# Optimization experiments

Hardware: AMD Instinct MI355X
Metric: run time of the kernel (lower is better)

## Reference

```python
import jax, jax.numpy as jnp
import numpy as np

E = 8192      # number of original edges -> artificial nodes
N = 2048      # number of original graph nodes (id range)
C_IN = 128
C_OUT = 128
NEG_SLOPE = 0.2


def setup_inputs() -> dict:
    key = jax.random.key(0)
    k1, k2, k3, k4, k5 = jax.random.split(key, 5)
    x = jax.random.normal(k1, (E, C_IN), dtype=jnp.float32)
    edge_index = jax.random.randint(k2, (2, E), 0, N, dtype=jnp.int64)
    # GATConv params (heads=1): linear weight, attention vectors, bias
    W = jax.random.normal(k3, (C_IN, C_OUT), dtype=jnp.float32) / np.sqrt(C_IN)
    att_src = jax.random.normal(k4, (C_OUT,), dtype=jnp.float32) / np.sqrt(C_OUT)
    att_dst = jax.random.normal(k5, (C_OUT,), dtype=jnp.float32) / np.sqrt(C_OUT)
    bias = jnp.zeros((C_OUT,), dtype=jnp.float32)
    return {"x": x, "edge_index": edge_index, "W": W,
            "att_src": att_src, "att_dst": att_dst, "bias": bias}


def reference(x, edge_index, W, att_src, att_dst, bias):
    # --- line-graph construction (vectorized version of the O(E^2) loop) ---
    s = edge_index[0]  # [E] source node of each original edge
    d = edge_index[1]  # [E] target node of each original edge
    share = ((s[:, None] == s[None, :]) | (s[:, None] == d[None, :]) |
             (d[:, None] == s[None, :]) | (d[:, None] == d[None, :]))  # [E,E]
    eye = jnp.eye(x.shape[0], dtype=bool)
    # original loop only adds pairs i != j (symmetrically); GATConv then adds self loops
    adj = (share & ~eye) | eye  # adj[i, j]: message j -> i allowed

    # --- GATConv (heads=1, concat) over the dense line-graph adjacency ---
    h = x @ W                       # [E, C_OUT]
    a_src = h @ att_src             # [E] per-source attention logit
    a_dst = h @ att_dst             # [E] per-target attention logit
    scores = a_dst[:, None] + a_src[None, :]          # [E,E], row=target, col=source
    scores = jax.nn.leaky_relu(scores, NEG_SLOPE)
    scores = jnp.where(adj, scores, -jnp.inf)
    alpha = jax.nn.softmax(scores, axis=1)            # softmax over source edges per target
    out = alpha @ h + bias          # [E, C_OUT]
    return out
```

## Files before the change

kernel.cpp:

```cpp
#include <hip/hip_runtime.h>

#define E 8192
#define NNODE 2048
#define C 128
#define CAPN 32
#define NIDX 8
#define NPI (NNODE / NIDX)
#define RPB 32
#define NGEMM (E / RPB)

typedef unsigned int u32;
typedef unsigned long long u64;

__global__ __launch_bounds__(256) void gat_prep(
    const float* __restrict__ x, const float* __restrict__ W,
    const float* __restrict__ att_s, const float* __restrict__ att_d,
    const float* __restrict__ bias, const int* __restrict__ ei,
    float* __restrict__ h, float* __restrict__ asrc, float* __restrict__ adst,
    int* __restrict__ packed, int* __restrict__ cnt, int* __restrict__ nlist)
{
    __shared__ __align__(16) float smem[8192];
    const int tid = threadIdx.x;

    if (blockIdx.x < NIDX) {
        int* lcnt = (int*)smem;
        const int lo = (int)blockIdx.x * NPI;
        if (tid < NPI) lcnt[tid] = 0;
        __syncthreads();
        for (int g = tid; g < E; g += 256) {
            const int s = ei[g], d = ei[E + g];
            if ((g >> 10) == (int)blockIdx.x)
                packed[g] = (s << 16) | d;
            const int sl = s - lo, dl = d - lo;
            if ((unsigned)sl < NPI) {
                const int slot = atomicAdd(&lcnt[sl], 1);
                if (slot < CAPN) nlist[s * CAPN + slot] = g;
            }
            if (d != s && (unsigned)dl < NPI) {
                const int slot = atomicAdd(&lcnt[dl], 1);
                if (slot < CAPN) nlist[d * CAPN + slot] = g;
            }
        }
        __syncthreads();
        if (tid < NPI) cnt[lo + tid] = lcnt[tid];
        return;
    }

    float* xs = smem;
    float* wt = smem + 4096;
    const int lane = tid & 63, wv = tid >> 6;
    const int row0 = ((int)blockIdx.x - NIDX) * RPB;

    #pragma unroll
    for (int u = 0; u < 4; ++u) {
        const int f = tid + u * 256;
        *reinterpret_cast<float4*>(&xs[f * 4]) =
            *reinterpret_cast<const float4*>(&x[(size_t)row0 * C + f * 4]);
    }

    float a0x = 0.f, a0y = 0.f, a1x = 0.f, a1y = 0.f;
    float a2x = 0.f, a2y = 0.f, a3x = 0.f, a3y = 0.f;
    float a4x = 0.f, a4y = 0.f, a5x = 0.f, a5y = 0.f;
    float a6x = 0.f, a6y = 0.f, a7x = 0.f, a7y = 0.f;
    const float* xw = xs + (wv * 8) * C;

    for (int kt = 0; kt < 4; ++kt) {
        __syncthreads();
        #pragma unroll
        for (int u = 0; u < 4; ++u) {
            const int f = tid + u * 256;
            *reinterpret_cast<float4*>(&wt[f * 4]) =
                *reinterpret_cast<const float4*>(&W[(size_t)kt * 32 * C + f * 4]);
        }
        __syncthreads();
        const int kb = kt * 32;
        #pragma unroll
        for (int k4 = 0; k4 < 8; ++k4) {
            float4 v0 = *reinterpret_cast<const float4*>(&xw[0 * C + kb + k4 * 4]);
            float4 v1 = *reinterpret_cast<const float4*>(&xw[1 * C + kb + k4 * 4]);
            float4 v2 = *reinterpret_cast<const float4*>(&xw[2 * C + kb + k4 * 4]);
            float4 v3 = *reinterpret_cast<const float4*>(&xw[3 * C + kb + k4 * 4]);
            float4 v4 = *reinterpret_cast<const float4*>(&xw[4 * C + kb + k4 * 4]);
            float4 v5 = *reinterpret_cast<const float4*>(&xw[5 * C + kb + k4 * 4]);
            float4 v6 = *reinterpret_cast<const float4*>(&xw[6 * C + kb + k4 * 4]);
            float4 v7 = *reinterpret_cast<const float4*>(&xw[7 * C + kb + k4 * 4]);
            const float2 w0 = *reinterpret_cast<const float2*>(&wt[(k4 * 4 + 0) * C + 2 * lane]);
            const float2 w1 = *reinterpret_cast<const float2*>(&wt[(k4 * 4 + 1) * C + 2 * lane]);
            const float2 w2 = *reinterpret_cast<const float2*>(&wt[(k4 * 4 + 2) * C + 2 * lane]);
            const float2 w3 = *reinterpret_cast<const float2*>(&wt[(k4 * 4 + 3) * C + 2 * lane]);
#define K4FMA(V, AX, AY)                                     \
            AX = fmaf(V.x, w0.x, AX); AY = fmaf(V.x, w0.y, AY); \
            AX = fmaf(V.y, w1.x, AX); AY = fmaf(V.y, w1.y, AY); \
            AX = fmaf(V.z, w2.x, AX); AY = fmaf(V.z, w2.y, AY); \
            AX = fmaf(V.w, w3.x, AX); AY = fmaf(V.w, w3.y, AY);
            K4FMA(v0, a0x, a0y) K4FMA(v1, a1x, a1y)
            K4FMA(v2, a2x, a2y) K4FMA(v3, a3x, a3y)
            K4FMA(v4, a4x, a4y) K4FMA(v5, a5x, a5y)
            K4FMA(v6, a6x, a6y) K4FMA(v7, a7x, a7y)
#undef K4FMA
        }
    }

    const float2 asv = *reinterpret_cast<const float2*>(att_s + 2 * lane);
    const float2 adv = *reinterpret_cast<const float2*>(att_d + 2 * lane);
    const float2 bv  = *reinterpret_cast<const float2*>(bias  + 2 * lane);
    const int rw0 = row0 + wv * 8;
#define EPI(R, AX, AY) {                                                        \
    *reinterpret_cast<float2*>(&h[(size_t)(rw0 + R) * C + 2 * lane]) =          \
        make_float2(AX + bv.x, AY + bv.y);              \
    float ps = fmaf(AX, asv.x, AY * asv.y);                                     \
    float pd = fmaf(AX, adv.x, AY * adv.y);                                     \
    _Pragma("unroll")                                                           \
    for (int off = 32; off > 0; off >>= 1) {                                    \
        ps += __shfl_xor(ps, off); pd += __shfl_xor(pd, off);                   \
    }                                                                           \
    if (lane == 0) { asrc[rw0 + R] = ps; adst[rw0 + R] = pd; } }
    EPI(0, a0x, a0y) EPI(1, a1x, a1y) EPI(2, a2x, a2y) EPI(3, a3x, a3y)
    EPI(4, a4x, a4y) EPI(5, a5x, a5y) EPI(6, a6x, a6y) EPI(7, a7x, a7y)
#undef EPI
}

__global__ __launch_bounds__(256) void gat_aggr(
    const int* __restrict__ packed, const float* __restrict__ h,
    const float* __restrict__ asrc, const float* __restrict__ adst,
    const int* __restrict__ cnt, const int* __restrict__ nlist,
    float* __restrict__ out)
{
    __shared__ float2 lst[4][64];
    const int tid = threadIdx.x, lane = tid & 63, wv = tid >> 6;
    const int i = blockIdx.x * 4 + wv;

    const u32 pi = (u32)packed[i];
    const int si = (int)(pi >> 16), di = (int)(pi & 0xffffu);
    const float adi = adst[i];
    int len_s = cnt[si]; if (len_s > CAPN) len_s = CAPN;
    int len_d = (di == si) ? 0 : cnt[di]; if (len_d > CAPN) len_d = CAPN;
    const int ntot = len_s + len_d;

    int key = 0x7fffffff;
    float sc = -INFINITY;
    bool valid = false;
    if (lane < ntot) {
        const bool from_s = lane < len_s;
        const int j = nlist[(from_s ? si : di) * CAPN + (from_s ? lane : lane - len_s)];
        const u32 pj = (u32)packed[j];
        valid = from_s || ((int)(pj >> 16) != si && (int)(pj & 0xffffu) != si);
        if (valid) {
            const float s0 = adi + asrc[j];
            sc = s0 >= 0.f ? s0 : 0.2f * s0;
            key = j;
        }
    }

    float m = sc;
    #pragma unroll
    for (int off = 32; off > 0; off >>= 1) m = fmaxf(m, __shfl_xor(m, off));
    const int nvalid = (int)__popcll(__ballot(valid));

    float p = __expf(sc - m);

    #pragma unroll
    for (int k = 2; k <= 64; k <<= 1) {
        #pragma unroll
        for (int st = k >> 1; st > 0; st >>= 1) {
            const int   ok = __shfl_xor(key, st);
            const float op = __shfl_xor(p, st);
            const bool takeMin = ((lane & k) == 0) == ((lane & st) == 0);
            if (takeMin ? (ok < key) : (ok > key)) { key = ok; p = op; }
        }
    }
    lst[wv][lane] = make_float2(__int_as_float(key == 0x7fffffff ? i : key), p);

    const int nch = (nvalid + 3) >> 2;
    float lsum = 0.f, o0 = 0.f, o1 = 0.f;
    const float* hb = h + 2 * lane;
    for (int t = 0; t < nch; ++t) {
        const float2 e0 = lst[wv][4 * t + 0];
        const float2 e1 = lst[wv][4 * t + 1];
        const float2 e2 = lst[wv][4 * t + 2];
        const float2 e3 = lst[wv][4 * t + 3];
        const float2 h0 = *reinterpret_cast<const float2*>(hb + (size_t)__float_as_int(e0.x) * C);
        const float2 h1 = *reinterpret_cast<const float2*>(hb + (size_t)__float_as_int(e1.x) * C);
        const float2 h2 = *reinterpret_cast<const float2*>(hb + (size_t)__float_as_int(e2.x) * C);
        const float2 h3 = *reinterpret_cast<const float2*>(hb + (size_t)__float_as_int(e3.x) * C);
        lsum += (e0.y + e1.y) + (e2.y + e3.y);
        o0 = fmaf(e0.y, h0.x, o0); o1 = fmaf(e0.y, h0.y, o1);
        o0 = fmaf(e1.y, h1.x, o0); o1 = fmaf(e1.y, h1.y, o1);
        o0 = fmaf(e2.y, h2.x, o0); o1 = fmaf(e2.y, h2.y, o1);
        o0 = fmaf(e3.y, h3.x, o0); o1 = fmaf(e3.y, h3.y, o1);
    }
    const float inv = 1.0f / lsum;
    *reinterpret_cast<float2*>(&out[(size_t)i * C + 2 * lane]) =
        make_float2(o0 * inv, o1 * inv);
}

extern "C" void kernel_launch(void* const* d_in, const int* in_sizes, int n_in,
                              void* d_out, int out_size, void* d_ws, size_t ws_size,
                              hipStream_t stream) {
    const float* x     = (const float*)d_in[0];
    const int*   ei    = (const int*)d_in[1];
    const float* W     = (const float*)d_in[2];
    const float* att_s = (const float*)d_in[3];
    const float* att_d = (const float*)d_in[4];
    const float* bias  = (const float*)d_in[5];

    float* h      = (float*)d_ws;
    float* asrc   = h + (size_t)E * C;
    float* adst   = asrc + E;
    int*   packed = (int*)(adst + E);
    int*   cnt    = packed + E;
    int*   nlist  = cnt + NNODE;

    gat_prep<<<NIDX + NGEMM, 256, 0, stream>>>(x, W, att_s, att_d, bias, ei,
                                               h, asrc, adst, packed, cnt, nlist);
    gat_aggr<<<E / 4, 256, 0, stream>>>(packed, h, asrc, adst, cnt, nlist,
                                        (float*)d_out);
}
```

Baseline: 45.20 us.

## Halve rows per GEMM block and stream W from global instead of LDS

The prep GEMM now handles 16 rows per block instead of 32, so twice as many blocks are launched and each wave owns 4 rows instead of 8. The K-tiled staging of W into shared memory, with its barriers, is removed, and W is read directly from global memory, relying on L2/L1 caching. This cuts LDS use and synchronisation and raises parallelism. In exchange, W reuse per block halves and global/cache traffic for W grows.

```diff
diff --git a/kernel.cpp b/kernel.cpp
--- a/kernel.cpp
+++ b/kernel.cpp
@@ -6,7 +6,7 @@
 #define CAPN 32
 #define NIDX 8
 #define NPI (NNODE / NIDX)
-#define RPB 32
+#define RPB 16
 #define NGEMM (E / RPB)
 
 typedef unsigned int u32;
@@ -19,7 +19,7 @@
     float* __restrict__ h, float* __restrict__ asrc, float* __restrict__ adst,
     int* __restrict__ packed, int* __restrict__ cnt, int* __restrict__ nlist)
 {
-    __shared__ __align__(16) float smem[8192];
+    __shared__ __align__(16) float smem[RPB * C];
     const int tid = threadIdx.x;
 
     if (blockIdx.x < NIDX) {
@@ -46,65 +46,46 @@
         return;
     }
 
-    float* xs = smem;
-    float* wt = smem + 4096;
     const int lane = tid & 63, wv = tid >> 6;
     const int row0 = ((int)blockIdx.x - NIDX) * RPB;
 
-    #pragma unroll
-    for (int u = 0; u < 4; ++u) {
-        const int f = tid + u * 256;
-        *reinterpret_cast<float4*>(&xs[f * 4]) =
-            *reinterpret_cast<const float4*>(&x[(size_t)row0 * C + f * 4]);
+    {
+        const float4* xg = reinterpret_cast<const float4*>(x + (size_t)row0 * C);
+        float4* xsv = reinterpret_cast<float4*>(smem);
+        xsv[tid]       = xg[tid];
+        xsv[tid + 256] = xg[tid + 256];
     }
+    __syncthreads();
 
     float a0x = 0.f, a0y = 0.f, a1x = 0.f, a1y = 0.f;
     float a2x = 0.f, a2y = 0.f, a3x = 0.f, a3y = 0.f;
-    float a4x = 0.f, a4y = 0.f, a5x = 0.f, a5y = 0.f;
-    float a6x = 0.f, a6y = 0.f, a7x = 0.f, a7y = 0.f;
-    const float* xw = xs + (wv * 8) * C;
+    const float* xw = smem + (wv * 4) * C;
+    const float* Wc = W + 2 * lane;
 
-    for (int kt = 0; kt < 4; ++kt) {
-        __syncthreads();
-        #pragma unroll
-        for (int u = 0; u < 4; ++u) {
-            const int f = tid + u * 256;
-            *reinterpret_cast<float4*>(&wt[f * 4]) =
-                *reinterpret_cast<const float4*>(&W[(size_t)kt * 32 * C + f * 4]);
-        }
-        __syncthreads();
-        const int kb = kt * 32;
-        #pragma unroll
-        for (int k4 = 0; k4 < 8; ++k4) {
-            float4 v0 = *reinterpret_cast<const float4*>(&xw[0 * C + kb + k4 * 4]);
-            float4 v1 = *reinterpret_cast<const float4*>(&xw[1 * C + kb + k4 * 4]);
-            float4 v2 = *reinterpret_cast<const float4*>(&xw[2 * C + kb + k4 * 4]);
-            float4 v3 = *reinterpret_cast<const float4*>(&xw[3 * C + kb + k4 * 4]);
-            float4 v4 = *reinterpret_cast<const float4*>(&xw[4 * C + kb + k4 * 4]);
-            float4 v5 = *reinterpret_cast<const float4*>(&xw[5 * C + kb + k4 * 4]);
-            float4 v6 = *reinterpret_cast<const float4*>(&xw[6 * C + kb + k4 * 4]);
-            float4 v7 = *reinterpret_cast<const float4*>(&xw[7 * C + kb + k4 * 4]);
-            const float2 w0 = *reinterpret_cast<const float2*>(&wt[(k4 * 4 + 0) * C + 2 * lane]);
-            const float2 w1 = *reinterpret_cast<const float2*>(&wt[(k4 * 4 + 1) * C + 2 * lane]);
-            const float2 w2 = *reinterpret_cast<const float2*>(&wt[(k4 * 4 + 2) * C + 2 * lane]);
-            const float2 w3 = *reinterpret_cast<const float2*>(&wt[(k4 * 4 + 3) * C + 2 * lane]);
-#define K4FMA(V, AX, AY)                                     \
-            AX = fmaf(V.x, w0.x, AX); AY = fmaf(V.x, w0.y, AY); \
-            AX = fmaf(V.y, w1.x, AX); AY = fmaf(V.y, w1.y, AY); \
-            AX = fmaf(V.z, w2.x, AX); AY = fmaf(V.z, w2.y, AY); \
-            AX = fmaf(V.w, w3.x, AX); AY = fmaf(V.w, w3.y, AY);
-            K4FMA(v0, a0x, a0y) K4FMA(v1, a1x, a1y)
-            K4FMA(v2, a2x, a2y) K4FMA(v3, a3x, a3y)
-            K4FMA(v4, a4x, a4y) K4FMA(v5, a5x, a5y)
-            K4FMA(v6, a6x, a6y) K4FMA(v7, a7x, a7y)
+    #pragma unroll 4
+    for (int k4 = 0; k4 < C / 4; ++k4) {
+        const float4 v0 = *reinterpret_cast<const float4*>(xw + 0 * C + 4 * k4);
+        const float4 v1 = *reinterpret_cast<const float4*>(xw + 1 * C + 4 * k4);
+        const float4 v2 = *reinterpret_cast<const float4*>(xw + 2 * C + 4 * k4);
+        const float4 v3 = *reinterpret_cast<const float4*>(xw + 3 * C + 4 * k4);
+        const float2 w0 = *reinterpret_cast<const float2*>(Wc + (4 * k4 + 0) * C);
+        const float2 w1 = *reinterpret_cast<const float2*>(Wc + (4 * k4 + 1) * C);
+        const float2 w2 = *reinterpret_cast<const float2*>(Wc + (4 * k4 + 2) * C);
+        const float2 w3 = *reinterpret_cast<const float2*>(Wc + (4 * k4 + 3) * C);
+#define K4FMA(V, AX, AY)                                        \
+        AX = fmaf(V.x, w0.x, AX); AY = fmaf(V.x, w0.y, AY);     \
+        AX = fmaf(V.y, w1.x, AX); AY = fmaf(V.y, w1.y, AY);     \
+        AX = fmaf(V.z, w2.x, AX); AY = fmaf(V.z, w2.y, AY);     \
+        AX = fmaf(V.w, w3.x, AX); AY = fmaf(V.w, w3.y, AY);
+        K4FMA(v0, a0x, a0y) K4FMA(v1, a1x, a1y)
+        K4FMA(v2, a2x, a2y) K4FMA(v3, a3x, a3y)
 #undef K4FMA
-        }
     }
 
     const float2 asv = *reinterpret_cast<const float2*>(att_s + 2 * lane);
     const float2 adv = *reinterpret_cast<const float2*>(att_d + 2 * lane);
     const float2 bv  = *reinterpret_cast<const float2*>(bias  + 2 * lane);
-    const int rw0 = row0 + wv * 8;
+    const int rw0 = row0 + wv * 4;
 #define EPI(R, AX, AY) {                                                        \
     *reinterpret_cast<float2*>(&h[(size_t)(rw0 + R) * C + 2 * lane]) =          \
         make_float2(AX + bv.x, AY + bv.y);              \
@@ -116,7 +97,6 @@
     }                                                                           \
     if (lane == 0) { asrc[rw0 + R] = ps; adst[rw0 + R] = pd; } }
     EPI(0, a0x, a0y) EPI(1, a1x, a1y) EPI(2, a2x, a2y) EPI(3, a3x, a3y)
-    EPI(4, a4x, a4y) EPI(5, a5x, a5y) EPI(6, a6x, a6y) EPI(7, a7x, a7y)
 #undef EPI
 }
 
```

After: 47.64 us. +5.4%, slower.
